# Kernel tuning notes

Measured on AMD Instinct MI355X. Metric: run time of the kernel, lower is better.

Reference implementation:

```python
import jax, jax.numpy as jnp
import numpy as np

D_MODEL, N_HEADS, D_FF = 768, 12, 3072
B, T = 4, 2048
EPS = 1e-5


def setup_inputs() -> dict:
    key = jax.random.key(0)
    ks = jax.random.split(key, 12)
    s = 0.02
    inp = {
        'x': jax.random.normal(ks[0], (B, T, D_MODEL), jnp.float32),
        'mask': jnp.tril(jnp.ones((1, 1, T, T), jnp.bool_)),  # causal decoder mask
        'ln1_g': jnp.ones((D_MODEL,), jnp.float32),
        'ln1_b': jnp.zeros((D_MODEL,), jnp.float32),
        'Wq': jax.random.normal(ks[1], (D_MODEL, D_MODEL), jnp.float32) * s,
        'bq': jnp.zeros((D_MODEL,), jnp.float32),
        'Wk': jax.random.normal(ks[2], (D_MODEL, D_MODEL), jnp.float32) * s,
        'bk': jnp.zeros((D_MODEL,), jnp.float32),
        'Wv': jax.random.normal(ks[3], (D_MODEL, D_MODEL), jnp.float32) * s,
        'bv': jnp.zeros((D_MODEL,), jnp.float32),
        'Wo': jax.random.normal(ks[4], (D_MODEL, D_MODEL), jnp.float32) * s,
        'bo': jnp.zeros((D_MODEL,), jnp.float32),
        'ln2_g': jnp.ones((D_MODEL,), jnp.float32),
        'ln2_b': jnp.zeros((D_MODEL,), jnp.float32),
        'W1': jax.random.normal(ks[5], (D_MODEL, D_FF), jnp.float32) * s,
        'b1': jnp.zeros((D_FF,), jnp.float32),
        'W2': jax.random.normal(ks[6], (D_FF, D_MODEL), jnp.float32) * s,
        'b2': jnp.zeros((D_MODEL,), jnp.float32),
    }
    return inp


def _layer_norm(x, g, b):
    mu = jnp.mean(x, axis=-1, keepdims=True)
    var = jnp.mean(jnp.square(x - mu), axis=-1, keepdims=True)
    return (x - mu) * jax.lax.rsqrt(var + EPS) * g + b


def reference(x, mask, ln1_g, ln1_b, Wq, bq, Wk, bk, Wv, bv, Wo, bo,
              ln2_g, ln2_b, W1, b1, W2, b2):
    Bx, Tx, _ = x.shape
    d_k = D_MODEL // N_HEADS
    # --- attention sublayer (pre-norm) ---
    h = _layer_norm(x, ln1_g, ln1_b)
    q = (h @ Wq + bq).reshape(Bx, Tx, N_HEADS, d_k).transpose(0, 2, 1, 3)
    k = (h @ Wk + bk).reshape(Bx, Tx, N_HEADS, d_k).transpose(0, 2, 1, 3)
    v = (h @ Wv + bv).reshape(Bx, Tx, N_HEADS, d_k).transpose(0, 2, 1, 3)
    scores = jnp.einsum('bhqd,bhkd->bhqk', q, k) / jnp.sqrt(jnp.float32(d_k))
    scores = jnp.where(mask, scores, -jnp.inf)
    weights = jax.nn.softmax(scores, axis=-1)
    attn = jnp.einsum('bhqk,bhkd->bhqd', weights, v)
    attn = attn.transpose(0, 2, 1, 3).reshape(Bx, Tx, D_MODEL)
    x = x + (attn @ Wo + bo)
    # --- FFN sublayer (pre-norm) ---
    h = _layer_norm(x, ln2_g, ln2_b)
    h = jax.nn.gelu(h @ W1 + b1, approximate=False)
    return x + (h @ W2 + b2)
```

## Files before the change

kernel.cpp:

```cpp
#include <hip/hip_runtime.h>

#define DEV __device__ __forceinline__

typedef __attribute__((ext_vector_type(8))) short short8;
typedef __attribute__((ext_vector_type(4))) float f32x4;
typedef __attribute__((ext_vector_type(16))) float f32x16;
typedef __attribute__((ext_vector_type(4))) unsigned int u32x4;
typedef __attribute__((ext_vector_type(2))) unsigned int u32x2;
typedef __attribute__((ext_vector_type(4))) unsigned short u16x4;

constexpr int Bc = 4, Tc = 2048, Dm = 768, Hh = 12, DK = 64, DFF = 3072;
constexpr int MT = Bc * Tc;

DEV unsigned short f2bf(float f) {
  unsigned int u = __float_as_uint(f);
  u += 0x7fff + ((u >> 16) & 1);
  return (unsigned short)(u >> 16);
}

DEV unsigned cvt_pk_bf16(float lo, float hi) {
  unsigned r;
  asm("v_cvt_pk_bf16_f32 %0, %1, %2" : "=v"(r) : "v"(lo), "v"(hi));
  return r;
}

DEV float gelu_fast(float v) {
  float y = 1.5957691216f * (v + 0.044715f * v * v * v);
  return v * (1.0f / (1.0f + __expf(-y)));
}

DEV void gload_lds16(const void* g, void* l) {
  __builtin_amdgcn_global_load_lds(
      (const __attribute__((address_space(1))) void*)g,
      (__attribute__((address_space(3))) void*)l, 16, 0, 0);
}

__global__ __launch_bounds__(256) void ln_kernel(const float* __restrict__ x,
    const float* __restrict__ gam, const float* __restrict__ bet,
    unsigned short* __restrict__ out)
{
  int lane = threadIdx.x & 63;
  int row = blockIdx.x * 4 + (threadIdx.x >> 6);
  const float* xr = x + (size_t)row * Dm + lane * 12;
  f32x4 v0 = *(const f32x4*)(xr);
  f32x4 v1 = *(const f32x4*)(xr + 4);
  f32x4 v2 = *(const f32x4*)(xr + 8);
  float s = 0.f, s2 = 0.f;
#pragma unroll
  for (int j = 0; j < 4; j++) {
    s  += v0[j] + v1[j] + v2[j];
    s2 += v0[j]*v0[j] + v1[j]*v1[j] + v2[j]*v2[j];
  }
#pragma unroll
  for (int off = 32; off; off >>= 1) { s += __shfl_xor(s, off); s2 += __shfl_xor(s2, off); }
  float mu = s * (1.f / Dm);
  float inv = rsqrtf(s2 * (1.f / Dm) - mu * mu + 1e-5f);
  int cb = lane * 12;
  unsigned short o[12];
#pragma unroll
  for (int j = 0; j < 4; j++) {
    o[j]     = f2bf((v0[j] - mu) * inv * gam[cb + j]     + bet[cb + j]);
    o[4 + j] = f2bf((v1[j] - mu) * inv * gam[cb + 4 + j] + bet[cb + 4 + j]);
    o[8 + j] = f2bf((v2[j] - mu) * inv * gam[cb + 8 + j] + bet[cb + 8 + j]);
  }
  unsigned short* orow = out + (size_t)row * Dm + cb;
#pragma unroll
  for (int i = 0; i < 3; i++) *(u16x4*)(orow + i * 4) = *(const u16x4*)(&o[i * 4]);
}

__global__ __launch_bounds__(256) void wtrans_all_kernel(
    const float* __restrict__ Wq, const float* __restrict__ Wk,
    const float* __restrict__ Wv, const float* __restrict__ Wo,
    const float* __restrict__ W1, const float* __restrict__ W2,
    unsigned short* wq_t, unsigned short* wk_t, unsigned short* wv_t,
    unsigned short* wo_t, unsigned short* w1_t, unsigned short* w2_t)
{
  __shared__ unsigned short tile[32][33];
  int bid = blockIdx.x;
  const float* src; unsigned short* dst; int K, N, t;
  if (bid < 2304) {
    int w = bid / 576; t = bid % 576; K = Dm; N = Dm;
    src = w == 0 ? Wq : w == 1 ? Wk : w == 2 ? Wv : Wo;
    dst = w == 0 ? wq_t : w == 1 ? wk_t : w == 2 ? wv_t : wo_t;
  } else if (bid < 4608) {
    t = bid - 2304; K = Dm; N = DFF; src = W1; dst = w1_t;
  } else {
    t = bid - 4608; K = DFF; N = Dm; src = W2; dst = w2_t;
  }
  int gx = N / 32;
  int n0 = (t % gx) * 32, k0 = (t / gx) * 32;
  int tx = threadIdx.x & 31, ty = threadIdx.x >> 5;
#pragma unroll
  for (int i = 0; i < 4; i++) {
    int kr = ty * 4 + i;
    tile[kr][tx] = f2bf(src[(size_t)(k0 + kr) * N + n0 + tx]);
  }
  __syncthreads();
#pragma unroll
  for (int i = 0; i < 4; i++) {
    int nr = ty * 4 + i;
    dst[(size_t)(n0 + nr) * K + k0 + tx] = tile[tx][nr];
  }
}

template<int OUT_MODE, bool SWAP>
DEV void gemm_body(unsigned short* As, unsigned short* Bs,
    const unsigned short* __restrict__ A, const unsigned short* __restrict__ Bt,
    const float* __restrict__ bias, const float* __restrict__ resid, void* __restrict__ out,
    int M, int N, int K)
{
  int m0 = blockIdx.x * 128, n0 = blockIdx.y * 128;
  int tid = threadIdx.x, lane = tid & 63, wid = tid >> 6;
  int wr = wid >> 1, wc = wid & 1;
  int r32 = lane & 31, l5 = lane >> 5;
  const unsigned short* pA[4]; const unsigned short* pB[4];
  unsigned short* dA[4]; unsigned short* dB[4];
#pragma unroll
  for (int p = 0; p < 4; p++) {
    int L = wid * 256 + p * 64 + lane;
    int row = L >> 3, pos = L & 7;
    int ch = pos ^ (row & 7);
    pA[p] = A + (size_t)(m0 + row) * K + ch * 8;
    pB[p] = Bt + (size_t)(n0 + row) * K + ch * 8;
    dA[p] = As + (size_t)L * 8;
    dB[p] = Bs + (size_t)L * 8;
  }
  f32x16 acc[2][2] = {};
  for (int k0 = 0; k0 < K; k0 += 64) {
    __syncthreads();
#pragma unroll
    for (int p = 0; p < 4; p++) {
      gload_lds16(pA[p] + k0, dA[p]);
      gload_lds16(pB[p] + k0, dB[p]);
    }
    __syncthreads();
#pragma unroll
    for (int kk = 0; kk < 4; kk++) {
      short8 af[2], bfr[2];
#pragma unroll
      for (int g = 0; g < 2; g++) {
        int rowA = wr * 64 + g * 32 + r32;
        af[g]  = *(const short8*)(&As[rowA * 64 + (((kk * 2 + l5) ^ (rowA & 7)) << 3)]);
        int rowB = wc * 64 + g * 32 + r32;
        bfr[g] = *(const short8*)(&Bs[rowB * 64 + (((kk * 2 + l5) ^ (rowB & 7)) << 3)]);
      }
#pragma unroll
      for (int mg = 0; mg < 2; mg++)
#pragma unroll
        for (int ng = 0; ng < 2; ng++) {
          if (SWAP)
            acc[mg][ng] = __builtin_amdgcn_mfma_f32_32x32x16_bf16(bfr[ng], af[mg], acc[mg][ng], 0, 0, 0);
          else
            acc[mg][ng] = __builtin_amdgcn_mfma_f32_32x32x16_bf16(af[mg], bfr[ng], acc[mg][ng], 0, 0, 0);
        }
    }
  }
  if (SWAP) {
#pragma unroll
    for (int mg = 0; mg < 2; mg++) {
      int gm = m0 + wr * 64 + mg * 32 + r32;
#pragma unroll
      for (int ng = 0; ng < 2; ng++) {
        int nbase = n0 + wc * 64 + ng * 32;
#pragma unroll
        for (int rq = 0; rq < 4; rq++) {
          int gn0 = nbase + rq * 8 + l5 * 4;
          f32x4 v;
#pragma unroll
          for (int rr = 0; rr < 4; rr++) v[rr] = acc[mg][ng][rq * 4 + rr];
          f32x4 bv = *(const f32x4*)(bias + gn0);
#pragma unroll
          for (int rr = 0; rr < 4; rr++) v[rr] += bv[rr];
          if (OUT_MODE == 2) {
#pragma unroll
            for (int rr = 0; rr < 4; rr++) v[rr] = gelu_fast(v[rr]);
          }
          if (OUT_MODE == 0) {
            f32x4 rv = *(const f32x4*)(resid + (size_t)gm * N + gn0);
#pragma unroll
            for (int rr = 0; rr < 4; rr++) v[rr] += rv[rr];
            *(f32x4*)(&((float*)out)[(size_t)gm * N + gn0]) = v;
          } else {
            u32x2 pk;
            pk[0] = cvt_pk_bf16(v[0], v[1]);
            pk[1] = cvt_pk_bf16(v[2], v[3]);
            if (OUT_MODE == 3) {
              int b = gm >> 11, tt = gm & 2047, h = gn0 >> 6, d = gn0 & 63;
              *(u32x2*)(&((unsigned short*)out)[(((size_t)b * Hh + h) * Tc + tt) * DK + d]) = pk;
            } else {
              *(u32x2*)(&((unsigned short*)out)[(size_t)gm * N + gn0]) = pk;
            }
          }
        }
      }
    }
  } else {
#pragma unroll
    for (int mg = 0; mg < 2; mg++) {
#pragma unroll
      for (int ng = 0; ng < 2; ng++) {
        int gn = n0 + wc * 64 + ng * 32 + r32;
        float bv = bias[gn];
        int h = gn >> 6, d = gn & 63;
#pragma unroll
        for (int rq = 0; rq < 4; rq++) {
          int gm0 = m0 + wr * 64 + mg * 32 + rq * 8 + l5 * 4;
          int b = gm0 >> 11, tt = gm0 & 2047;
          u16x4 pk;
#pragma unroll
          for (int rr = 0; rr < 4; rr++) pk[rr] = f2bf(acc[mg][ng][rq * 4 + rr] + bv);
          *(u16x4*)(&((unsigned short*)out)[(((size_t)b * Hh + h) * DK + d) * Tc + tt]) = pk;
        }
      }
    }
  }
}

__global__ __launch_bounds__(256) void gemm_f32out_kernel(const unsigned short* A,
    const unsigned short* Bt, const float* bias, const float* resid, float* out,
    int M, int N, int K)
{
  __shared__ unsigned short As[128 * 64], Bs[128 * 64];
  gemm_body<0, true>(As, Bs, A, Bt, bias, resid, out, M, N, K);
}

__global__ __launch_bounds__(256) void gemm_gelu_kernel(const unsigned short* A,
    const unsigned short* Bt, const float* bias, unsigned short* out,
    int M, int N, int K)
{
  __shared__ unsigned short As[128 * 64], Bs[128 * 64];
  gemm_body<2, true>(As, Bs, A, Bt, bias, nullptr, out, M, N, K);
}

__global__ __launch_bounds__(256) void gemm_qkv_kernel(const unsigned short* A,
    const unsigned short* Bq, const unsigned short* Bk, const unsigned short* Bv,
    const float* bq, const float* bk, const float* bv,
    unsigned short* oq, unsigned short* okh, unsigned short* ovt)
{
  __shared__ unsigned short As[128 * 64], Bs[128 * 64];
  if (blockIdx.z == 0)      gemm_body<1, true >(As, Bs, A, Bq, bq, nullptr, oq,  MT, Dm, Dm);
  else if (blockIdx.z == 1) gemm_body<3, true >(As, Bs, A, Bk, bk, nullptr, okh, MT, Dm, Dm);
  else                      gemm_body<4, false>(As, Bs, A, Bv, bv, nullptr, ovt, MT, Dm, Dm);
}

__global__ __launch_bounds__(256) void attn_kernel(const unsigned short* __restrict__ q,
    const unsigned short* __restrict__ kh, const unsigned short* __restrict__ vt,
    unsigned short* __restrict__ o)
{
  __shared__ unsigned short Ks[2][64 * 64], Vs[2][64 * 64];
  __shared__ unsigned short P_lds[4][16 * 64];
  int lane = threadIdx.x & 63, wid = threadIdx.x >> 6;
  int fr = lane & 15, fg = lane >> 4;
  int bid = blockIdx.x;
  int xcd = bid & 7, ii = bid >> 3;
  int bh = xcd * 6 + (ii >> 5);
  int qc = 31 - (ii & 31);
  int b = bh / Hh, h = bh - b * Hh;
  int q0 = qc * 64 + wid * 16;
  const size_t qbase = ((size_t)b * Tc) * Dm + h * DK;
  const unsigned short* kg = kh + (size_t)bh * Tc * DK;
  const unsigned short* vg = vt + (size_t)bh * DK * Tc;
  const unsigned short* pK[2]; const unsigned short* pV[2];
  int ldsoff[2];
#pragma unroll
  for (int c = 0; c < 2; c++) {
    int L = c * 256 + wid * 64 + lane;
    int row = L >> 3, cc = (L & 7) ^ (row & 7);
    pK[c] = kg + (size_t)row * DK + cc * 8;
    pV[c] = vg + (size_t)row * Tc + cc * 8;
    ldsoff[c] = L * 8;
  }
  short8 qa0 = *(const short8*)(&q[qbase + (size_t)(q0 + fr) * Dm + fg * 8]);
  short8 qa1 = *(const short8*)(&q[qbase + (size_t)(q0 + fr) * Dm + 32 + fg * 8]);
  f32x4 oa[4] = {};
  f32x4 rs = {};
  short8 onesb;
#pragma unroll
  for (int j = 0; j < 8; j++) onesb[j] = (short)0x3F80;
  unsigned short* Pw = P_lds[wid];
  int nIter = qc + 1;

#define STAGE(buf, kk0)                                                          \
  {                                                                              \
    _Pragma("unroll")                                                            \
    for (int c = 0; c < 2; c++) {                                                \
      gload_lds16(pK[c] + (size_t)(kk0) * DK, &Ks[buf][ldsoff[c]]);              \
      gload_lds16(pV[c] + (kk0),              &Vs[buf][ldsoff[c]]);              \
    }                                                                            \
  }

  STAGE(0, 0)
  for (int it = 0; it < nIter; it++) {
    int cur = it & 1;
    if (it + 1 < nIter) {
      STAGE(cur ^ 1, (it + 1) * 64)
      asm volatile("s_waitcnt vmcnt(4)" ::: "memory");
    } else {
      asm volatile("s_waitcnt vmcnt(0)" ::: "memory");
    }
    __builtin_amdgcn_s_barrier();
    int k0 = it * 64;
    f32x4 st[4];
#pragma unroll
    for (int t = 0; t < 4; t++) {
      int row = t * 16 + fr;
      short8 kf0 = *(const short8*)(&Ks[cur][row * 64 + ((fg)     ^ (fr & 7)) * 8]);
      short8 kf1 = *(const short8*)(&Ks[cur][row * 64 + ((4 + fg) ^ (fr & 7)) * 8]);
      st[t] = {};
      st[t] = __builtin_amdgcn_mfma_f32_16x16x32_bf16(kf0, qa0, st[t], 0, 0, 0);
      st[t] = __builtin_amdgcn_mfma_f32_16x16x32_bf16(kf1, qa1, st[t], 0, 0, 0);
    }
    short8 vb[4][2];
#pragma unroll
    for (int dg = 0; dg < 4; dg++) {
      int row = dg * 16 + fr;
#pragma unroll
      for (int hf = 0; hf < 2; hf++)
        vb[dg][hf] = *(const short8*)(&Vs[cur][row * 64 + ((hf * 4 + fg) ^ (fr & 7)) * 8]);
    }
    bool masked = (it == nIter - 1);
#pragma unroll
    for (int t = 0; t < 4; t++) {
      float p[4];
#pragma unroll
      for (int rr = 0; rr < 4; rr++) {
        float e = __expf(st[t][rr] * 0.125f);
        if (masked) {
          int key = k0 + t * 16 + fg * 4 + rr;
          e = (key <= q0 + fr) ? e : 0.f;
        }
        p[rr] = e;
      }
      u32x2 pkw;
      pkw[0] = cvt_pk_bf16(p[0], p[1]);
      pkw[1] = cvt_pk_bf16(p[2], p[3]);
      int C = t * 2 + (fg >> 1);
      *(u32x2*)(&Pw[fr * 64 + ((C ^ (fr & 7)) << 3) + ((fg & 1) << 2)]) = pkw;
    }
    asm volatile("s_waitcnt lgkmcnt(0)" ::: "memory");
    __builtin_amdgcn_sched_barrier(0);
    short8 pa0 = *(const short8*)(&Pw[fr * 64 + ((fg     ^ (fr & 7)) * 8)]);
    short8 pa1 = *(const short8*)(&Pw[fr * 64 + (((4 + fg) ^ (fr & 7)) * 8)]);
    rs = __builtin_amdgcn_mfma_f32_16x16x32_bf16(pa0, onesb, rs, 0, 0, 0);
    rs = __builtin_amdgcn_mfma_f32_16x16x32_bf16(pa1, onesb, rs, 0, 0, 0);
#pragma unroll
    for (int dg = 0; dg < 4; dg++) {
      oa[dg] = __builtin_amdgcn_mfma_f32_16x16x32_bf16(pa0, vb[dg][0], oa[dg], 0, 0, 0);
      oa[dg] = __builtin_amdgcn_mfma_f32_16x16x32_bf16(pa1, vb[dg][1], oa[dg], 0, 0, 0);
    }
    __builtin_amdgcn_s_barrier();
  }
#undef STAGE
  f32x4 rinv;
#pragma unroll
  for (int rr = 0; rr < 4; rr++) rinv[rr] = __builtin_amdgcn_rcpf(rs[rr]);
#pragma unroll
  for (int dg = 0; dg < 4; dg++)
#pragma unroll
    for (int rr = 0; rr < 4; rr++) {
      int qi = q0 + fg * 4 + rr;
      o[qbase + (size_t)qi * Dm + dg * 16 + fr] = f2bf(oa[dg][rr] * rinv[rr]);
    }
}

extern "C" void kernel_launch(void* const* d_in, const int* in_sizes, int n_in,
                              void* d_out, int out_size, void* d_ws, size_t ws_size,
                              hipStream_t stream) {
  const float* x     = (const float*)d_in[0];
  const float* ln1_g = (const float*)d_in[2];
  const float* ln1_b = (const float*)d_in[3];
  const float* Wq = (const float*)d_in[4];  const float* bq = (const float*)d_in[5];
  const float* Wk = (const float*)d_in[6];  const float* bk = (const float*)d_in[7];
  const float* Wv = (const float*)d_in[8];  const float* bv = (const float*)d_in[9];
  const float* Wo = (const float*)d_in[10]; const float* bo = (const float*)d_in[11];
  const float* ln2_g = (const float*)d_in[12];
  const float* ln2_b = (const float*)d_in[13];
  const float* W1 = (const float*)d_in[14]; const float* b1 = (const float*)d_in[15];
  const float* W2 = (const float*)d_in[16]; const float* b2 = (const float*)d_in[17];
  float* out = (float*)d_out;

  char* ws = (char*)d_ws;
  const size_t HB = (size_t)MT * Dm * 2;
  unsigned short* h_buf  = (unsigned short*)(ws);
  unsigned short* q_buf  = (unsigned short*)(ws + HB);
  unsigned short* kh_buf = (unsigned short*)(ws + 2 * HB);
  unsigned short* vt_buf = (unsigned short*)(ws + 3 * HB);
  unsigned short* wq_t   = (unsigned short*)(ws + 4 * HB);
  unsigned short* wk_t   = wq_t + (size_t)Dm * Dm;
  unsigned short* wv_t   = wk_t + (size_t)Dm * Dm;
  unsigned short* wo_t   = wv_t + (size_t)Dm * Dm;
  unsigned short* w1_t   = wo_t + (size_t)Dm * Dm;
  unsigned short* w2_t   = w1_t + (size_t)Dm * DFF;
  unsigned short* g_buf  = w2_t + (size_t)DFF * Dm;

  wtrans_all_kernel<<<dim3(6912), 256, 0, stream>>>(
      Wq, Wk, Wv, Wo, W1, W2, wq_t, wk_t, wv_t, wo_t, w1_t, w2_t);

  ln_kernel<<<MT / 4, 256, 0, stream>>>(x, ln1_g, ln1_b, h_buf);
  gemm_qkv_kernel<<<dim3(MT / 128, Dm / 128, 3), 256, 0, stream>>>(
      h_buf, wq_t, wk_t, wv_t, bq, bk, bv, q_buf, kh_buf, vt_buf);
  attn_kernel<<<dim3(1536), 256, 0, stream>>>(q_buf, kh_buf, vt_buf, h_buf);
  gemm_f32out_kernel<<<dim3(MT / 128, Dm / 128), 256, 0, stream>>>(
      h_buf, wo_t, bo, x, out, MT, Dm, Dm);
  ln_kernel<<<MT / 4, 256, 0, stream>>>(out, ln2_g, ln2_b, h_buf);
  gemm_gelu_kernel<<<dim3(MT / 128, DFF / 128), 256, 0, stream>>>(
      h_buf, w1_t, b1, g_buf, MT, DFF, Dm);
  gemm_f32out_kernel<<<dim3(MT / 128, Dm / 128), 256, 0, stream>>>(
      g_buf, w2_t, b2, out, out, MT, Dm, DFF);
}
```

Before: 272.0 us.

## Double-buffer GEMM LDS tiles to overlap global loads with MFMA compute

Gives the shared GEMM body two LDS buffers for the A and B tiles. The next K-tile is issued with global-to-LDS loads before computing on the current one, which removes one of the two barriers per iteration. This is meant to hide global load latency behind the MFMA work. In exchange, LDS use per block doubles to 64KB, which may lower occupancy. The single barrier relies on the async LDS loads having completed by the end of each iteration.

```diff
diff --git a/kernel.cpp b/kernel.cpp
--- a/kernel.cpp
+++ b/kernel.cpp
@@ -125,24 +125,34 @@
     dA[p] = As + (size_t)L * 8;
     dB[p] = Bs + (size_t)L * 8;
   }
+  const int nT = K >> 6;
   f32x16 acc[2][2] = {};
-  for (int k0 = 0; k0 < K; k0 += 64) {
-    __syncthreads();
-#pragma unroll
-    for (int p = 0; p < 4; p++) {
-      gload_lds16(pA[p] + k0, dA[p]);
-      gload_lds16(pB[p] + k0, dB[p]);
-    }
-    __syncthreads();
+
+#define STAGE_G(c, koff)                                                        \
+  {                                                                             \
+    _Pragma("unroll")                                                           \
+    for (int p = 0; p < 4; p++) {                                               \
+      gload_lds16(pA[p] + (koff), dA[p] + (c) * 8192);                          \
+      gload_lds16(pB[p] + (koff), dB[p] + (c) * 8192);                          \
+    }                                                                           \
+  }
+
+  STAGE_G(0, 0)
+  __syncthreads();
+  int cur = 0;
+  for (int t = 0; t < nT; t++) {
+    if (t + 1 < nT) STAGE_G(cur ^ 1, (t + 1) * 64)
+    const unsigned short* Ac = As + cur * 8192;
+    const unsigned short* Bc = Bs + cur * 8192;
 #pragma unroll
     for (int kk = 0; kk < 4; kk++) {
       short8 af[2], bfr[2];
 #pragma unroll
       for (int g = 0; g < 2; g++) {
         int rowA = wr * 64 + g * 32 + r32;
-        af[g]  = *(const short8*)(&As[rowA * 64 + (((kk * 2 + l5) ^ (rowA & 7)) << 3)]);
+        af[g]  = *(const short8*)(&Ac[rowA * 64 + (((kk * 2 + l5) ^ (rowA & 7)) << 3)]);
         int rowB = wc * 64 + g * 32 + r32;
-        bfr[g] = *(const short8*)(&Bs[rowB * 64 + (((kk * 2 + l5) ^ (rowB & 7)) << 3)]);
+        bfr[g] = *(const short8*)(&Bc[rowB * 64 + (((kk * 2 + l5) ^ (rowB & 7)) << 3)]);
       }
 #pragma unroll
       for (int mg = 0; mg < 2; mg++)
@@ -154,7 +164,10 @@
             acc[mg][ng] = __builtin_amdgcn_mfma_f32_32x32x16_bf16(af[mg], bfr[ng], acc[mg][ng], 0, 0, 0);
         }
     }
-  }
+    __syncthreads();
+    cur ^= 1;
+  }
+#undef STAGE_G
   if (SWAP) {
 #pragma unroll
     for (int mg = 0; mg < 2; mg++) {
@@ -220,7 +233,7 @@
     const unsigned short* Bt, const float* bias, const float* resid, float* out,
     int M, int N, int K)
 {
-  __shared__ unsigned short As[128 * 64], Bs[128 * 64];
+  __shared__ unsigned short As[2 * 128 * 64], Bs[2 * 128 * 64];
   gemm_body<0, true>(As, Bs, A, Bt, bias, resid, out, M, N, K);
 }
 
@@ -228,7 +241,7 @@
     const unsigned short* Bt, const float* bias, unsigned short* out,
     int M, int N, int K)
 {
-  __shared__ unsigned short As[128 * 64], Bs[128 * 64];
+  __shared__ unsigned short As[2 * 128 * 64], Bs[2 * 128 * 64];
   gemm_body<2, true>(As, Bs, A, Bt, bias, nullptr, out, M, N, K);
 }
 
@@ -237,7 +250,7 @@
     const float* bq, const float* bk, const float* bv,
     unsigned short* oq, unsigned short* okh, unsigned short* ovt)
 {
-  __shared__ unsigned short As[128 * 64], Bs[128 * 64];
+  __shared__ unsigned short As[2 * 128 * 64], Bs[2 * 128 * 64];
   if (blockIdx.z == 0)      gemm_body<1, true >(As, Bs, A, Bq, bq, nullptr, oq,  MT, Dm, Dm);
   else if (blockIdx.z == 1) gemm_body<3, true >(As, Bs, A, Bk, bk, nullptr, okh, MT, Dm, Dm);
   else                      gemm_body<4, false>(As, Bs, A, Bv, bv, nullptr, ovt, MT, Dm, Dm);
```

After: 278.1 us. 2.2% more time.

## Switch GEMMs to single-wave 64x64 tiles with triple-buffered async LDS pipeline

Applied to the files above, without the earlier changes.

Replaces the 4-wave 128x128 GEMM tile with a one-wave 64x64 tile per block. The K loop now runs a 3-stage LDS ring buffer that uses vmcnt/lgkmcnt waits instead of __syncthreads. The aim is to overlap global-to-LDS loads with MFMA work and remove barrier stalls. In exchange, each block loses tile reuse: global/L2 traffic per FLOP doubles and there are many more, smaller blocks.

```diff
diff --git a/kernel.cpp b/kernel.cpp
--- a/kernel.cpp
+++ b/kernel.cpp
@@ -104,20 +104,19 @@
 }
 
 template<int OUT_MODE, bool SWAP>
-DEV void gemm_body(unsigned short* As, unsigned short* Bs,
+DEV void gemm1w_body(unsigned short* As, unsigned short* Bs,
     const unsigned short* __restrict__ A, const unsigned short* __restrict__ Bt,
     const float* __restrict__ bias, const float* __restrict__ resid, void* __restrict__ out,
     int M, int N, int K)
 {
-  int m0 = blockIdx.x * 128, n0 = blockIdx.y * 128;
-  int tid = threadIdx.x, lane = tid & 63, wid = tid >> 6;
-  int wr = wid >> 1, wc = wid & 1;
+  int m0 = blockIdx.x * 64, n0 = blockIdx.y * 64;
+  int lane = threadIdx.x & 63;
   int r32 = lane & 31, l5 = lane >> 5;
-  const unsigned short* pA[4]; const unsigned short* pB[4];
-  unsigned short* dA[4]; unsigned short* dB[4];
-#pragma unroll
-  for (int p = 0; p < 4; p++) {
-    int L = wid * 256 + p * 64 + lane;
+  const unsigned short* pA[8]; const unsigned short* pB[8];
+  unsigned short* dA[8]; unsigned short* dB[8];
+#pragma unroll
+  for (int p = 0; p < 8; p++) {
+    int L = p * 64 + lane;
     int row = L >> 3, pos = L & 7;
     int ch = pos ^ (row & 7);
     pA[p] = A + (size_t)(m0 + row) * K + ch * 8;
@@ -125,24 +124,41 @@
     dA[p] = As + (size_t)L * 8;
     dB[p] = Bs + (size_t)L * 8;
   }
+  const int nT = K >> 6;
   f32x16 acc[2][2] = {};
-  for (int k0 = 0; k0 < K; k0 += 64) {
-    __syncthreads();
-#pragma unroll
-    for (int p = 0; p < 4; p++) {
-      gload_lds16(pA[p] + k0, dA[p]);
-      gload_lds16(pB[p] + k0, dB[p]);
-    }
-    __syncthreads();
+
+#define STAGE1(c, koff)                                                        \
+  {                                                                            \
+    _Pragma("unroll")                                                          \
+    for (int p = 0; p < 8; p++) {                                              \
+      gload_lds16(pA[p] + (koff), dA[p] + (c) * 4096);                         \
+      gload_lds16(pB[p] + (koff), dB[p] + (c) * 4096);                         \
+    }                                                                          \
+  }
+
+  STAGE1(0, 0)
+  STAGE1(1, 64)
+  for (int t = 0; t < nT; t++) {
+    if (t + 2 < nT) {
+      asm volatile("s_waitcnt lgkmcnt(0)" ::: "memory");
+      STAGE1((t + 2) % 3, (t + 2) * 64)
+      asm volatile("s_waitcnt vmcnt(32)" ::: "memory");
+    } else if (t + 1 < nT) {
+      asm volatile("s_waitcnt vmcnt(16)" ::: "memory");
+    } else {
+      asm volatile("s_waitcnt vmcnt(0)" ::: "memory");
+    }
+    const unsigned short* Ac = As + (size_t)(t % 3) * 4096;
+    const unsigned short* Bcc = Bs + (size_t)(t % 3) * 4096;
 #pragma unroll
     for (int kk = 0; kk < 4; kk++) {
       short8 af[2], bfr[2];
 #pragma unroll
       for (int g = 0; g < 2; g++) {
-        int rowA = wr * 64 + g * 32 + r32;
-        af[g]  = *(const short8*)(&As[rowA * 64 + (((kk * 2 + l5) ^ (rowA & 7)) << 3)]);
-        int rowB = wc * 64 + g * 32 + r32;
-        bfr[g] = *(const short8*)(&Bs[rowB * 64 + (((kk * 2 + l5) ^ (rowB & 7)) << 3)]);
+        int rowA = g * 32 + r32;
+        af[g]  = *(const short8*)(&Ac[rowA * 64 + (((kk * 2 + l5) ^ (rowA & 7)) << 3)]);
+        int rowB = g * 32 + r32;
+        bfr[g] = *(const short8*)(&Bcc[rowB * 64 + (((kk * 2 + l5) ^ (rowB & 7)) << 3)]);
       }
 #pragma unroll
       for (int mg = 0; mg < 2; mg++)
@@ -155,13 +171,14 @@
         }
     }
   }
+#undef STAGE1
   if (SWAP) {
 #pragma unroll
     for (int mg = 0; mg < 2; mg++) {
-      int gm = m0 + wr * 64 + mg * 32 + r32;
+      int gm = m0 + mg * 32 + r32;
 #pragma unroll
       for (int ng = 0; ng < 2; ng++) {
-        int nbase = n0 + wc * 64 + ng * 32;
+        int nbase = n0 + ng * 32;
 #pragma unroll
         for (int rq = 0; rq < 4; rq++) {
           int gn0 = nbase + rq * 8 + l5 * 4;
@@ -199,12 +216,12 @@
     for (int mg = 0; mg < 2; mg++) {
 #pragma unroll
       for (int ng = 0; ng < 2; ng++) {
-        int gn = n0 + wc * 64 + ng * 32 + r32;
+        int gn = n0 + ng * 32 + r32;
         float bv = bias[gn];
         int h = gn >> 6, d = gn & 63;
 #pragma unroll
         for (int rq = 0; rq < 4; rq++) {
-          int gm0 = m0 + wr * 64 + mg * 32 + rq * 8 + l5 * 4;
+          int gm0 = m0 + mg * 32 + rq * 8 + l5 * 4;
           int b = gm0 >> 11, tt = gm0 & 2047;
           u16x4 pk;
 #pragma unroll
@@ -216,31 +233,31 @@
   }
 }
 
-__global__ __launch_bounds__(256) void gemm_f32out_kernel(const unsigned short* A,
+__global__ __launch_bounds__(64) void gemm_f32out_kernel(const unsigned short* A,
     const unsigned short* Bt, const float* bias, const float* resid, float* out,
     int M, int N, int K)
 {
-  __shared__ unsigned short As[128 * 64], Bs[128 * 64];
-  gemm_body<0, true>(As, Bs, A, Bt, bias, resid, out, M, N, K);
-}
-
-__global__ __launch_bounds__(256) void gemm_gelu_kernel(const unsigned short* A,
+  __shared__ unsigned short As[3 * 64 * 64], Bs[3 * 64 * 64];
+  gemm1w_body<0, true>(As, Bs, A, Bt, bias, resid, out, M, N, K);
+}
+
+__global__ __launch_bounds__(64) void gemm_gelu_kernel(const unsigned short* A,
     const unsigned short* Bt, const float* bias, unsigned short* out,
     int M, int N, int K)
 {
-  __shared__ unsigned short As[128 * 64], Bs[128 * 64];
-  gemm_body<2, true>(As, Bs, A, Bt, bias, nullptr, out, M, N, K);
-}
-
-__global__ __launch_bounds__(256) void gemm_qkv_kernel(const unsigned short* A,
+  __shared__ unsigned short As[3 * 64 * 64], Bs[3 * 64 * 64];
+  gemm1w_body<2, true>(As, Bs, A, Bt, bias, nullptr, out, M, N, K);
+}
+
+__global__ __launch_bounds__(64) void gemm_qkv_kernel(const unsigned short* A,
     const unsigned short* Bq, const unsigned short* Bk, const unsigned short* Bv,
     const float* bq, const float* bk, const float* bv,
     unsigned short* oq, unsigned short* okh, unsigned short* ovt)
 {
-  __shared__ unsigned short As[128 * 64], Bs[128 * 64];
-  if (blockIdx.z == 0)      gemm_body<1, true >(As, Bs, A, Bq, bq, nullptr, oq,  MT, Dm, Dm);
-  else if (blockIdx.z == 1) gemm_body<3, true >(As, Bs, A, Bk, bk, nullptr, okh, MT, Dm, Dm);
-  else                      gemm_body<4, false>(As, Bs, A, Bv, bv, nullptr, ovt, MT, Dm, Dm);
+  __shared__ unsigned short As[3 * 64 * 64], Bs[3 * 64 * 64];
+  if (blockIdx.z == 0)      gemm1w_body<1, true >(As, Bs, A, Bq, bq, nullptr, oq,  MT, Dm, Dm);
+  else if (blockIdx.z == 1) gemm1w_body<3, true >(As, Bs, A, Bk, bk, nullptr, okh, MT, Dm, Dm);
+  else                      gemm1w_body<4, false>(As, Bs, A, Bv, bv, nullptr, ovt, MT, Dm, Dm);
 }
 
 __global__ __launch_bounds__(256) void attn_kernel(const unsigned short* __restrict__ q,
@@ -397,14 +414,14 @@
       Wq, Wk, Wv, Wo, W1, W2, wq_t, wk_t, wv_t, wo_t, w1_t, w2_t);
 
   ln_kernel<<<MT / 4, 256, 0, stream>>>(x, ln1_g, ln1_b, h_buf);
-  gemm_qkv_kernel<<<dim3(MT / 128, Dm / 128, 3), 256, 0, stream>>>(
+  gemm_qkv_kernel<<<dim3(MT / 64, Dm / 64, 3), 64, 0, stream>>>(
       h_buf, wq_t, wk_t, wv_t, bq, bk, bv, q_buf, kh_buf, vt_buf);
   attn_kernel<<<dim3(1536), 256, 0, stream>>>(q_buf, kh_buf, vt_buf, h_buf);
-  gemm_f32out_kernel<<<dim3(MT / 128, Dm / 128), 256, 0, stream>>>(
+  gemm_f32out_kernel<<<dim3(MT / 64, Dm / 64), 64, 0, stream>>>(
       h_buf, wo_t, bo, x, out, MT, Dm, Dm);
   ln_kernel<<<MT / 4, 256, 0, stream>>>(out, ln2_g, ln2_b, h_buf);
-  gemm_gelu_kernel<<<dim3(MT / 128, DFF / 128), 256, 0, stream>>>(
+  gemm_gelu_kernel<<<dim3(MT / 64, DFF / 64), 64, 0, stream>>>(
       h_buf, w1_t, b1, g_buf, MT, DFF, Dm);
-  gemm_f32out_kernel<<<dim3(MT / 128, Dm / 128), 256, 0, stream>>>(
+  gemm_f32out_kernel<<<dim3(MT / 64, Dm / 64), 64, 0, stream>>>(
       g_buf, w2_t, b2, out, out, MT, Dm, DFF);
 }
```

After: 401.2 us. 47.5% more time.
